# Kernel tuning notes

Hardware: AMD Instinct MI355X
Metric: run time of the kernel (lower is better)

Reference implementation:

```python
import jax, jax.numpy as jnp
import numpy as np

IN_SZ = 256
OUT_SZ = 256
RANK = 60  # min(60, IN_SZ*OUT_SZ)
C = 512    # channel_size
N_SEL = 256
B = 1024


def setup_inputs() -> dict:
    key = jax.random.key(0)
    k_x, k_u, k_v, k_b, k_i = jax.random.split(key, 5)
    # match torch init scales: U ~ U(-sqrt(3/rank), ...), V ~ U(-sqrt(1/(in*out)),...)
    bu = np.sqrt(3.0 / RANK)
    bv = np.sqrt(1.0 / (IN_SZ * OUT_SZ))
    bb = np.sqrt(1.0 / RANK)
    x = jax.random.normal(k_x, (N_SEL, B, IN_SZ), dtype=jnp.float32)
    weights_U = jax.random.uniform(k_u, (C, RANK), jnp.float32, -bu, bu)
    weights_V = jax.random.uniform(k_v, (RANK, IN_SZ * OUT_SZ), jnp.float32, -bv, bv)
    bias = jax.random.uniform(k_b, (C, 1, OUT_SZ), jnp.float32, -bb, bb)
    indices = jax.random.randint(k_i, (N_SEL,), 0, C, dtype=jnp.int64)
    return {"x": x, "indices": indices, "weights_U": weights_U,
            "weights_V": weights_V, "bias": bias}


def reference(x, indices, weights_U, weights_V, bias):
    # Synthesize full per-channel weights, then gather selected channels
    # (faithful to the original: full U @ V materialized before gather).
    weight = (weights_U @ weights_V).reshape(-1, IN_SZ, OUT_SZ)  # [C, in, out]
    w = weight[indices]                                          # [n, in, out]
    # per-channel batched matmul: [n, B, in] x [n, in, out] -> [n, B, out]
    out = jnp.einsum('nbi,nio->nbo', x, w) + bias[indices]
    return out
```

## Files before the change

### kernel.cpp

```cpp
#include <hip/hip_runtime.h>
#include <hip/hip_bf16.h>
#include <stdint.h>

#define IN_SZ   256
#define OUT_SZ  256
#define RANK    60
#define NSEL    256
#define BATCH   1024
#define WELEMS  (IN_SZ * OUT_SZ)

typedef __attribute__((ext_vector_type(8))) short          short8;
typedef __attribute__((ext_vector_type(4))) float          f32x4;

static __device__ __forceinline__ unsigned short f32_to_bf16(float f) {
    union { float f; uint32_t u; } c; c.f = f;
    uint32_t u = c.u;
    u += 0x7fffu + ((u >> 16) & 1u);
    return (unsigned short)(u >> 16);
}

static __device__ __forceinline__ short8 cvt8(f32x4 lo, f32x4 hi) {
    union { short8 s; __hip_bfloat162 h[4]; } u;
    u.h[0] = __float22bfloat162_rn(make_float2(lo[0], lo[1]));
    u.h[1] = __float22bfloat162_rn(make_float2(lo[2], lo[3]));
    u.h[2] = __float22bfloat162_rn(make_float2(hi[0], hi[1]));
    u.h[3] = __float22bfloat162_rn(make_float2(hi[2], hi[3]));
    return u.s;
}

__global__ __launch_bounds__(256) void synth_w(
    const float* __restrict__ U, const float* __restrict__ V,
    const int* __restrict__ idx, unsigned short* __restrict__ wt)
{
    __shared__ unsigned short Cs[16][2064];

    int bid = blockIdx.x;
    int L   = (bid & 7) * 64 + (bid >> 3);
    int ic  = L >> 4;
    int g16 = L & 15;

    int tid = threadIdx.x, lane = tid & 63, wv = tid >> 6;

    int arow = lane & 15;
    int c    = idx[g16 * 16 + arow];
    short8 afr[2];
    #pragma unroll
    for (int ks = 0; ks < 2; ++ks) {
        short8 h;
        #pragma unroll
        for (int j = 0; j < 8; ++j) {
            int r = ks * 32 + (lane >> 4) * 8 + j;
            float u = (r < RANK) ? U[c * RANK + r] : 0.f;
            h[j] = (short)f32_to_bf16(u);
        }
        afr[ks] = h;
    }

    const float* Vb = V + (size_t)ic * 2048;
    #pragma unroll 2
    for (int mt = 0; mt < 32; ++mt) {
        int mloc = (wv * 32 + mt) * 16 + (lane & 15);
        f32x4 acc = {};
        #pragma unroll
        for (int ks = 0; ks < 2; ++ks) {
            short8 b;
            #pragma unroll
            for (int j = 0; j < 8; ++j) {
                int r = ks * 32 + (lane >> 4) * 8 + j;
                float v = (r < RANK) ? Vb[(size_t)r * WELEMS + mloc] : 0.f;
                b[j] = (short)f32_to_bf16(v);
            }
            acc = __builtin_amdgcn_mfma_f32_16x16x32_bf16(afr[ks], b, acc, 0, 0, 0);
        }
        #pragma unroll
        for (int j = 0; j < 4; ++j) {
            int nl = (lane >> 4) * 4 + j;
            Cs[nl][wv * 512 + mt * 16 + (lane & 15)] = f32_to_bf16(acc[j]);
        }
    }
    __syncthreads();

    #pragma unroll
    for (int t0 = 0; t0 < 16; ++t0) {
        int t  = t0 * 256 + tid;
        int nl = t >> 8;
        int o  = t & 255;
        short8 h;
        #pragma unroll
        for (int il = 0; il < 8; ++il) h[il] = (short)Cs[nl][il * 256 + o];
        int n = g16 * 16 + nl;
        size_t base = (size_t)n * WELEMS + (size_t)ic * 2048 + (size_t)o * 8;
        *reinterpret_cast<short8*>(wt + base) = h;
    }
}

__global__ __launch_bounds__(512, 2) void gemm_k(
    const float* __restrict__ x, const int* __restrict__ idx,
    const unsigned short* __restrict__ wt, const float* __restrict__ bias,
    float* __restrict__ out)
{
    __shared__ __align__(16) unsigned short Wl[WELEMS];
    __shared__ __align__(16) float          Bl[256];

    int n    = blockIdx.x;
    int tid  = threadIdx.x;
    int lane = tid & 63;
    int wv   = tid >> 6;
    int r16  = lane & 15;
    int q    = lane >> 4;

    const unsigned short* wn = wt + (size_t)n * WELEMS;

    #pragma unroll
    for (int j = 0; j < 16; ++j) {
        int g = wv * 16 + j;
        __builtin_amdgcn_global_load_lds(
            (const __attribute__((address_space(1))) void*)(wn + g * 512 + lane * 8),
            (__attribute__((address_space(3))) void*)(&Wl[g * 512]),
            16, 0, 0);
    }
    int c = idx[n];
    if (tid < 64) {
        f32x4 b = *reinterpret_cast<const f32x4*>(bias + (size_t)c * OUT_SZ + tid * 4);
        *reinterpret_cast<f32x4*>(&Bl[tid * 4]) = b;
    }
    __syncthreads();

    const float* xw = x + (size_t)n * (BATCH * IN_SZ)
                        + (size_t)(wv * 128 + r16) * IN_SZ + q * 8;
    float*       ow = out + (size_t)n * (BATCH * OUT_SZ)
                        + (size_t)(wv * 128 + r16) * OUT_SZ + q * 4;
    const char*  wl = reinterpret_cast<const char*>(Wl);
    int lq = q * 4096 + r16 * 16;

    f32x4 P0[4][2], P1[4][2];

    auto loadHalf = [&](f32x4 (&P)[4][2], int s) {
        const float* xp = xw + (size_t)(s >> 1) * 16 * IN_SZ + (s & 1) * 128;
        #pragma unroll
        for (int k = 0; k < 4; ++k) {
            P[k][0] = *reinterpret_cast<const f32x4*>(xp + k * 32);
            P[k][1] = *(reinterpret_cast<const f32x4*>(xp + k * 32) + 1);
        }
    };

    loadHalf(P0, 0);
    loadHalf(P1, 1);

    f32x4 acc[16];

    #pragma unroll
    for (int s = 0; s < 16; ++s) {
        if ((s & 1) == 0) {
            #pragma unroll
            for (int nf = 0; nf < 16; ++nf)
                acc[nf] = *reinterpret_cast<const f32x4*>(&Bl[nf * 16 + q * 4]);
        }

        f32x4 (&Pc)[4][2] = (s & 1) ? P1 : P0;

        #pragma unroll
        for (int k = 0; k < 4; ++k) {
            int ks = (s & 1) * 4 + k;
            short8 af = cvt8(Pc[k][0], Pc[k][1]);
            #pragma unroll
            for (int nf = 0; nf < 16; ++nf) {
                short8 bf = *reinterpret_cast<const short8*>(
                    wl + lq + ks * 16384 + nf * 256);
                acc[nf] = __builtin_amdgcn_mfma_f32_16x16x32_bf16(
                    bf, af, acc[nf], 0, 0, 0);
            }
        }

        if (s < 14) loadHalf((s & 1) ? P1 : P0, s + 2);

        if (s & 1) {
            float* op = ow + (size_t)(s >> 1) * 16 * OUT_SZ;
            #pragma unroll
            for (int nf = 0; nf < 16; ++nf)
                *reinterpret_cast<f32x4*>(op + nf * 16) = acc[nf];
        }
    }
}

extern "C" void kernel_launch(void* const* d_in, const int* in_sizes, int n_in,
                              void* d_out, int out_size, void* d_ws, size_t ws_size,
                              hipStream_t stream) {
    const float* x    = (const float*)d_in[0];
    const int*   idx  = (const int*)  d_in[1];
    const float* U    = (const float*)d_in[2];
    const float* V    = (const float*)d_in[3];
    const float* bias = (const float*)d_in[4];
    float* out = (float*)d_out;
    unsigned short* wt = (unsigned short*)d_ws;
    (void)in_sizes; (void)n_in; (void)out_size; (void)ws_size;

    synth_w<<<dim3(512), dim3(256), 0, stream>>>(U, V, idx, wt);
    gemm_k <<<dim3(256), dim3(512), 0, stream>>>(x, idx, wt, bias, out);
}
```

Measured before the change: 163.8 us.

## Split per-channel GEMM into 8 blocks holding weight fragments in registers

The GEMM kernel previously used one 512-thread block per selected channel, staging the full 256x256 bf16 weight matrix in LDS. It now launches 2048 blocks of 256 threads. Each block covers a quarter of the batch rows and half of the output columns, and each wave keeps its 32-column weight slice in registers, so LDS staging and the barrier go away. The trade-off is that each x row is now re-read from global memory by the two column-half blocks and by every wave within a block, which doubles or more the x traffic. Each wave also runs only two MFMAs per A fragment, which may leave the kernel memory- or latency-bound.

```diff
diff --git a/kernel.cpp b/kernel.cpp
--- a/kernel.cpp
+++ b/kernel.cpp
@@ -94,44 +94,47 @@
     }
 }
 
-__global__ __launch_bounds__(512, 2) void gemm_k(
+__global__ __launch_bounds__(256, 3) void gemm_k(
     const float* __restrict__ x, const int* __restrict__ idx,
     const unsigned short* __restrict__ wt, const float* __restrict__ bias,
     float* __restrict__ out)
 {
-    __shared__ __align__(16) unsigned short Wl[WELEMS];
-    __shared__ __align__(16) float          Bl[256];
+    int bid = blockIdx.x;
+    int L   = (bid & 7) * 256 + (bid >> 3);
+    int n   = L >> 3;
+    int sub = L & 7;
+    int cb  = sub & 1;
+    int rb  = sub >> 1;
 
-    int n    = blockIdx.x;
     int tid  = threadIdx.x;
     int lane = tid & 63;
     int wv   = tid >> 6;
     int r16  = lane & 15;
     int q    = lane >> 4;
 
-    const unsigned short* wn = wt + (size_t)n * WELEMS;
+    int col0 = cb * 128 + wv * 32;
 
+    const unsigned short* wq = wt + (size_t)n * WELEMS + q * 2048
+                                  + (size_t)(col0 + r16) * 8;
+    short8 B[8][2];
     #pragma unroll
-    for (int j = 0; j < 16; ++j) {
-        int g = wv * 16 + j;
-        __builtin_amdgcn_global_load_lds(
-            (const __attribute__((address_space(1))) void*)(wn + g * 512 + lane * 8),
-            (__attribute__((address_space(3))) void*)(&Wl[g * 512]),
-            16, 0, 0);
-    }
+    for (int ks = 0; ks < 8; ++ks)
+        #pragma unroll
+        for (int nf = 0; nf < 2; ++nf)
+            B[ks][nf] = *reinterpret_cast<const short8*>(
+                wq + (size_t)ks * 8192 + nf * 128);
+
     int c = idx[n];
-    if (tid < 64) {
-        f32x4 b = *reinterpret_cast<const f32x4*>(bias + (size_t)c * OUT_SZ + tid * 4);
-        *reinterpret_cast<f32x4*>(&Bl[tid * 4]) = b;
-    }
-    __syncthreads();
+    f32x4 bv[2];
+    #pragma unroll
+    for (int nf = 0; nf < 2; ++nf)
+        bv[nf] = *reinterpret_cast<const f32x4*>(
+            bias + (size_t)c * OUT_SZ + col0 + nf * 16 + q * 4);
 
     const float* xw = x + (size_t)n * (BATCH * IN_SZ)
-                        + (size_t)(wv * 128 + r16) * IN_SZ + q * 8;
+                        + (size_t)(rb * 256 + r16) * IN_SZ + q * 8;
     float*       ow = out + (size_t)n * (BATCH * OUT_SZ)
-                        + (size_t)(wv * 128 + r16) * OUT_SZ + q * 4;
-    const char*  wl = reinterpret_cast<const char*>(Wl);
-    int lq = q * 4096 + r16 * 16;
+                        + (size_t)(rb * 256 + r16) * OUT_SZ + col0 + q * 4;
 
     f32x4 P0[4][2], P1[4][2];
 
@@ -147,14 +150,13 @@
     loadHalf(P0, 0);
     loadHalf(P1, 1);
 
-    f32x4 acc[16];
+    f32x4 acc[2];
 
     #pragma unroll
-    for (int s = 0; s < 16; ++s) {
+    for (int s = 0; s < 32; ++s) {
         if ((s & 1) == 0) {
-            #pragma unroll
-            for (int nf = 0; nf < 16; ++nf)
-                acc[nf] = *reinterpret_cast<const f32x4*>(&Bl[nf * 16 + q * 4]);
+            acc[0] = bv[0];
+            acc[1] = bv[1];
         }
 
         f32x4 (&Pc)[4][2] = (s & 1) ? P1 : P0;
@@ -164,21 +166,17 @@
             int ks = (s & 1) * 4 + k;
             short8 af = cvt8(Pc[k][0], Pc[k][1]);
             #pragma unroll
-            for (int nf = 0; nf < 16; ++nf) {
-                short8 bf = *reinterpret_cast<const short8*>(
-                    wl + lq + ks * 16384 + nf * 256);
+            for (int nf = 0; nf < 2; ++nf)
                 acc[nf] = __builtin_amdgcn_mfma_f32_16x16x32_bf16(
-                    bf, af, acc[nf], 0, 0, 0);
-            }
+                    B[ks][nf], af, acc[nf], 0, 0, 0);
         }
 
-        if (s < 14) loadHalf((s & 1) ? P1 : P0, s + 2);
+        if (s < 30) loadHalf((s & 1) ? P1 : P0, s + 2);
 
         if (s & 1) {
             float* op = ow + (size_t)(s >> 1) * 16 * OUT_SZ;
-            #pragma unroll
-            for (int nf = 0; nf < 16; ++nf)
-                *reinterpret_cast<f32x4*>(op + nf * 16) = acc[nf];
+            *reinterpret_cast<f32x4*>(op)      = acc[0];
+            *reinterpret_cast<f32x4*>(op + 16) = acc[1];
         }
     }
 }
@@ -195,6 +193,6 @@
     unsigned short* wt = (unsigned short*)d_ws;
     (void)in_sizes; (void)n_in; (void)out_size; (void)ws_size;
 
-    synth_w<<<dim3(512), dim3(256), 0, stream>>>(U, V, idx, wt);
-    gemm_k <<<dim3(256), dim3(512), 0, stream>>>(x, idx, wt, bias, out);
+    synth_w<<<dim3(512),  dim3(256), 0, stream>>>(U, V, idx, wt);
+    gemm_k <<<dim3(2048), dim3(256), 0, stream>>>(x, idx, wt, bias, out);
 }
```

Result: slower. 303.7 us, median of 3 (+85.4%).
